# Kernel tuning notes

Hardware: AMD Instinct MI355X
Metric: run time of the kernel (lower is better)

## Reference

```python
import jax, jax.numpy as jnp
import numpy as np

N_NODES = 100000
N_EDGES = 1600000
N_GRAPHS = 512
IN_FEATS = 128
HIDDEN = 128
EXTRA = 8


def setup_inputs() -> dict:
    key = jax.random.key(0)
    ks = jax.random.split(key, 20)
    inp = {
        'feats_node': jax.random.normal(ks[0], (N_NODES, IN_FEATS), jnp.float32),
        'feats_graph': jax.random.normal(ks[1], (N_GRAPHS, EXTRA), jnp.float32),
        'edge_src': jax.random.randint(ks[2], (N_EDGES,), 0, N_NODES, jnp.int32),
        'edge_dst': jax.random.randint(ks[3], (N_EDGES,), 0, N_NODES, jnp.int32),
        'graph_ids': jnp.sort(jax.random.randint(ks[4], (N_NODES,), 0, N_GRAPHS, jnp.int32)),
        # GraphConv weights (in, out) and biases, init ~ N(0, 0.5^2) / zeros as in torch code
        'W1': 0.5 * jax.random.normal(ks[5], (IN_FEATS, HIDDEN), jnp.float32),
        'b1': jnp.zeros((HIDDEN,), jnp.float32),
        'W2': 0.5 * jax.random.normal(ks[6], (HIDDEN, HIDDEN), jnp.float32),
        'b2': jnp.zeros((HIDDEN,), jnp.float32),
        'W3': 0.5 * jax.random.normal(ks[7], (HIDDEN, HIDDEN), jnp.float32),
        'b3': jnp.zeros((HIDDEN,), jnp.float32),
        # MLP head
        'Wl1': 0.5 * jax.random.normal(ks[8], (HIDDEN + EXTRA, 2 * HIDDEN), jnp.float32),
        'bl1': jnp.zeros((2 * HIDDEN,), jnp.float32),
        'Wl2': 0.5 * jax.random.normal(ks[9], (2 * HIDDEN, HIDDEN), jnp.float32),
        'bl2': jnp.zeros((HIDDEN,), jnp.float32),
        'Wl3': 0.5 * jax.random.normal(ks[10], (HIDDEN, 1), jnp.float32),
        'bl3': jnp.zeros((1,), jnp.float32),
    }
    return inp


def _graph_conv(x, edge_src, edge_dst, norm_src, norm_dst, W, b):
    # DGL GraphConv, norm='both': D_dst^{-1/2} A D_src^{-1/2} X W + b
    h = x * norm_src[:, None]
    agg = jax.ops.segment_sum(h[edge_src], edge_dst, num_segments=N_NODES)
    agg = agg * norm_dst[:, None]
    return agg @ W + b


def reference(feats_node, feats_graph, edge_src, edge_dst, graph_ids,
              W1, b1, W2, b2, W3, b3, Wl1, bl1, Wl2, bl2, Wl3, bl3):
    ones_e = jnp.ones((N_EDGES,), jnp.float32)
    deg_out = jax.ops.segment_sum(ones_e, edge_src, num_segments=N_NODES)
    deg_in = jax.ops.segment_sum(ones_e, edge_dst, num_segments=N_NODES)
    norm_src = jnp.clip(deg_out, 1.0) ** -0.5  # out-degree norm on source side
    norm_dst = jnp.clip(deg_in, 1.0) ** -0.5   # in-degree norm on dest side

    x = jax.nn.selu(_graph_conv(feats_node, edge_src, edge_dst, norm_src, norm_dst, W1, b1))
    x = jax.nn.selu(_graph_conv(x, edge_src, edge_dst, norm_src, norm_dst, W2, b2))
    x = _graph_conv(x, edge_src, edge_dst, norm_src, norm_dst, W3, b3)

    # segment-mean readout per graph
    sums = jax.ops.segment_sum(x, graph_ids, num_segments=N_GRAPHS)
    counts = jax.ops.segment_sum(jnp.ones((N_NODES,), jnp.float32), graph_ids, num_segments=N_GRAPHS)
    embedding = sums / jnp.clip(counts, 1.0)[:, None]

    y = jnp.concatenate([embedding, feats_graph], axis=1)
    y = jax.nn.selu(y @ Wl1 + bl1)
    y = jax.nn.selu(y @ Wl2 + bl2)
    return (y @ Wl3 + bl3).reshape(-1)
```

## Files before the change

kernel.cpp:

```cpp
#include <hip/hip_runtime.h>
#include <hip/hip_fp16.h>
#include <math.h>

#define N_NODES   100000
#define N_EDGES   1600000
#define N_GRAPHS  512
#define FEAT      128
#define EXTRA     8

#define NB    196
#define PA_T  3072
#define PA_K  12

typedef _Float16 half8_t __attribute__((ext_vector_type(8)));
typedef float    f32x4_t __attribute__((ext_vector_type(4)));

static __device__ __forceinline__ float selu_f(float x){
    const float alpha = 1.6732632423543772f;
    const float scale = 1.0507009873554805f;
    return scale * (x > 0.0f ? x : alpha * expm1f(x));
}

__global__ void k_zero_i4(int4* __restrict__ p, int n4){
    int i = blockIdx.x*blockDim.x + threadIdx.x;
    if (i < n4) p[i] = make_int4(0,0,0,0);
}

__global__ __launch_bounds__(256) void k_bhist2(
        const int* __restrict__ esrc, const int* __restrict__ edst,
        int* __restrict__ bh_src, int* __restrict__ bh_dst){
    __shared__ int lhs[NB];
    __shared__ int lhd[NB];
    for (int i = threadIdx.x; i < NB; i += 256){ lhs[i] = 0; lhd[i] = 0; }
    __syncthreads();
    int stride = gridDim.x * blockDim.x;
    for (int e = blockIdx.x*blockDim.x + threadIdx.x; e < N_EDGES; e += stride){
        atomicAdd(&lhs[esrc[e] >> 9], 1);
        atomicAdd(&lhd[edst[e] >> 9], 1);
    }
    __syncthreads();
    for (int i = threadIdx.x; i < NB; i += 256){
        if (lhs[i]) atomicAdd(&bh_src[i], lhs[i]);
        if (lhd[i]) atomicAdd(&bh_dst[i], lhd[i]);
    }
}

__global__ void k_bscan2(const int* __restrict__ bh_dst, int* __restrict__ bbase,
                         int* __restrict__ gcursor, int* __restrict__ row_ptr,
                         const int* __restrict__ bh_src, int* __restrict__ sbase,
                         int* __restrict__ scursor){
    if (threadIdx.x == 0 && blockIdx.x == 0){
        int run = 0;
        for (int i = 0; i < NB; ++i){ bbase[i] = run; gcursor[i] = run; run += bh_dst[i]; }
        bbase[NB] = run;
        row_ptr[N_NODES] = N_EDGES;
        run = 0;
        for (int i = 0; i < NB; ++i){ sbase[i] = run; scursor[i] = run; run += bh_src[i]; }
        sbase[NB] = run;
    }
}

__global__ __launch_bounds__(256) void k_passA(
        const int* __restrict__ esrc, const int* __restrict__ edst,
        int* __restrict__ gcursor, uint2* __restrict__ tmp){
    __shared__ int   lcount[NB];
    __shared__ int   lscan[256];
    __shared__ int   gbase[NB];
    __shared__ ushort bid[PA_T];
    __shared__ uint2 staged[PA_T];
    __shared__ int   Vtot;
    int t = threadIdx.x;
    int base = blockIdx.x * PA_T;
    for (int i = t; i < NB; i += 256) lcount[i] = 0;
    __syncthreads();
    int bk[PA_K], slot[PA_K]; uint2 pr[PA_K];
    #pragma unroll
    for (int k = 0; k < PA_K; ++k){
        int e = base + k*256 + t;
        if (e < N_EDGES){
            int d = edst[e];
            int s = esrc[e];
            int b = d >> 9;
            bk[k] = b;
            pr[k] = make_uint2((unsigned)d, (unsigned)s);
            slot[k] = atomicAdd(&lcount[b], 1);
        } else bk[k] = -1;
    }
    __syncthreads();
    int v = (t < NB) ? lcount[t] : 0;
    lscan[t] = v;
    __syncthreads();
    for (int d = 1; d < 256; d <<= 1){
        int u = (t >= d) ? lscan[t-d] : 0;
        __syncthreads();
        lscan[t] += u;
        __syncthreads();
    }
    int excl = lscan[t] - v;
    if (t < NB) gbase[t] = atomicAdd(&gcursor[t], v);
    __syncthreads();
    lscan[t] = excl;
    if (t == 255) Vtot = excl + v;
    __syncthreads();
    #pragma unroll
    for (int k = 0; k < PA_K; ++k){
        if (bk[k] >= 0){
            int i = lscan[bk[k]] + slot[k];
            staged[i] = pr[k];
            bid[i] = (ushort)bk[k];
        }
    }
    __syncthreads();
    int total = Vtot;
    for (int i = t; i < total; i += 256){
        int b = bid[i];
        tmp[gbase[b] + (i - lscan[b])] = staged[i];
    }
}

__global__ __launch_bounds__(256) void k_passA_src(
        const int* __restrict__ esrc, int* __restrict__ scursor,
        ushort* __restrict__ tmp2){
    __shared__ int    lcount[NB];
    __shared__ int    lscan[256];
    __shared__ int    gbase[NB];
    __shared__ ushort bid[PA_T];
    __shared__ ushort staged[PA_T];
    __shared__ int    Vtot;
    int t = threadIdx.x;
    int base = blockIdx.x * PA_T;
    for (int i = t; i < NB; i += 256) lcount[i] = 0;
    __syncthreads();
    int bk[PA_K], slot[PA_K]; ushort pv[PA_K];
    #pragma unroll
    for (int k = 0; k < PA_K; ++k){
        int e = base + k*256 + t;
        if (e < N_EDGES){
            int s = esrc[e];
            int b = s >> 9;
            bk[k] = b;
            pv[k] = (ushort)(s & 511);
            slot[k] = atomicAdd(&lcount[b], 1);
        } else bk[k] = -1;
    }
    __syncthreads();
    int v = (t < NB) ? lcount[t] : 0;
    lscan[t] = v;
    __syncthreads();
    for (int d = 1; d < 256; d <<= 1){
        int u = (t >= d) ? lscan[t-d] : 0;
        __syncthreads();
        lscan[t] += u;
        __syncthreads();
    }
    int excl = lscan[t] - v;
    if (t < NB) gbase[t] = atomicAdd(&scursor[t], v);
    __syncthreads();
    lscan[t] = excl;
    if (t == 255) Vtot = excl + v;
    __syncthreads();
    #pragma unroll
    for (int k = 0; k < PA_K; ++k){
        if (bk[k] >= 0){
            int i = lscan[bk[k]] + slot[k];
            staged[i] = pv[k];
            bid[i] = (ushort)bk[k];
        }
    }
    __syncthreads();
    int total = Vtot;
    for (int i = t; i < total; i += 256){
        int b = bid[i];
        tmp2[gbase[b] + (i - lscan[b])] = staged[i];
    }
}

__global__ __launch_bounds__(256) void k_srchist(
        const ushort* __restrict__ tmp2, const int* __restrict__ sbase,
        float* __restrict__ ns){
    __shared__ int hc[512];
    int b = blockIdx.x, t = threadIdx.x;
    int node0 = b << 9;
    int lo = sbase[b], hi = sbase[b+1];
    hc[t] = 0; hc[t+256] = 0;
    __syncthreads();
    for (int p = lo + t; p < hi; p += 256)
        atomicAdd(&hc[tmp2[p]], 1);
    __syncthreads();
    int n0 = node0 + t, n1 = n0 + 256;
    if (n0 < N_NODES){ int c = hc[t];     ns[n0] = rsqrtf((float)(c > 1 ? c : 1)); }
    if (n1 < N_NODES){ int c = hc[t+256]; ns[n1] = rsqrtf((float)(c > 1 ? c : 1)); }
}

__global__ __launch_bounds__(256) void k_passB(
        const uint2* __restrict__ tmp, const int* __restrict__ bbase,
        int* __restrict__ row_ptr, int* __restrict__ col, float* __restrict__ nd){
    __shared__ int hc[512];
    __shared__ int hs[512];
    int b = blockIdx.x, t = threadIdx.x;
    int node0 = b << 9;
    int lo = bbase[b], hi = bbase[b+1];
    hc[t] = 0; hc[t+256] = 0;
    __syncthreads();
    for (int p = lo + t; p < hi; p += 256){
        int d = (int)tmp[p].x;
        atomicAdd(&hc[d - node0], 1);
    }
    __syncthreads();
    int a0 = hc[2*t], a1 = hc[2*t+1];
    int s = a0 + a1;
    hs[t] = s;
    __syncthreads();
    for (int d = 1; d < 256; d <<= 1){
        int u = (t >= d) ? hs[t-d] : 0;
        __syncthreads();
        hs[t] += u;
        __syncthreads();
    }
    int excl = hs[t] - s;
    __syncthreads();
    hs[2*t]   = excl;
    hs[2*t+1] = excl + a0;
    int n0 = node0 + 2*t, n1 = n0 + 1;
    if (n0 < N_NODES){
        row_ptr[n0] = lo + excl;
        nd[n0] = rsqrtf((float)(a0 > 1 ? a0 : 1));
    }
    if (n1 < N_NODES){
        row_ptr[n1] = lo + excl + a0;
        nd[n1] = rsqrtf((float)(a1 > 1 ? a1 : 1));
    }
    __syncthreads();
    for (int p = lo + t; p < hi; p += 256){
        uint2 e = tmp[p];
        int slot = atomicAdd(&hs[(int)e.x - node0], 1);
        col[lo + slot] = (int)e.y;
    }
}

__global__ void k_prep(const float2* __restrict__ x2, const float* __restrict__ ns,
                       __half2* __restrict__ xh2){
    int i = blockIdx.x*blockDim.x + threadIdx.x;
    if (i < N_NODES*64){
        int node = i >> 6;
        float w = ns[node];
        float2 v = x2[i];
        xh2[i] = __floats2half2_rn(v.x*w, v.y*w);
    }
}

__global__ void k_wprep(const float* __restrict__ W, __half* __restrict__ Wf){
    int i = blockIdx.x*256 + threadIdx.x;
    if (i >= 16384) return;
    int j = i & 7, lane = (i>>3) & 63, kk = (i>>9) & 3, c = i>>11;
    int k = kk*32 + ((lane>>4)<<3) + j;
    int cc = (c<<4) + (lane & 15);
    Wf[i] = __float2half(W[k*FEAT + cc]);
}

__global__ __launch_bounds__(256) void k_aggregate_h(
        const __half* __restrict__ xh, const int* __restrict__ row_ptr,
        const int* __restrict__ col, const float* __restrict__ nd,
        __half* __restrict__ outh){
    int gid  = blockIdx.x*blockDim.x + threadIdx.x;
    int node = gid >> 6;
    if (node >= N_NODES) return;
    int lane = threadIdx.x & 63;
    int sub  = lane >> 4;
    int fl   = lane & 15;
    int beg = row_ptr[node], end = row_ptr[node+1];

    float acc[8] = {0,0,0,0,0,0,0,0};
    for (int eb = beg; eb < end; eb += 16){
        int idx[4];
        uint4 r[4];
        #pragma unroll
        for (int j = 0; j < 4; ++j){
            int e = eb + 4*j + sub;
            idx[j] = (e < end) ? col[e] : -1;
        }
        #pragma unroll
        for (int j = 0; j < 4; ++j){
            r[j] = (idx[j] >= 0)
                 ? *(const uint4*)(xh + (size_t)idx[j]*FEAT + fl*8)
                 : make_uint4(0u,0u,0u,0u);
        }
        #pragma unroll
        for (int j = 0; j < 4; ++j){
            const __half2* h = (const __half2*)&r[j];
            #pragma unroll
            for (int q = 0; q < 4; ++q){
                float2 f = __half22float2(h[q]);
                acc[2*q]   += f.x;
                acc[2*q+1] += f.y;
            }
        }
    }
    #pragma unroll
    for (int q = 0; q < 8; ++q){
        acc[q] += __shfl_xor(acc[q], 16, 64);
        acc[q] += __shfl_xor(acc[q], 32, 64);
    }
    if (lane < 16){
        float wd = nd[node];
        union { __half2 h[4]; uint4 u; } pk;
        pk.h[0] = __floats2half2_rn(acc[0]*wd, acc[1]*wd);
        pk.h[1] = __floats2half2_rn(acc[2]*wd, acc[3]*wd);
        pk.h[2] = __floats2half2_rn(acc[4]*wd, acc[5]*wd);
        pk.h[3] = __floats2half2_rn(acc[6]*wd, acc[7]*wd);
        *(uint4*)(outh + (size_t)node*FEAT + fl*8) = pk.u;
    }
}

template<int ACT, int HALF_OUT>
__global__ __launch_bounds__(256) void k_gemm_mfma(
        const __half* __restrict__ A, const __half* __restrict__ Wf,
        const float* __restrict__ bias, const float* __restrict__ ns,
        float* __restrict__ fout, __half* __restrict__ hout){
    int w = threadIdx.x >> 6, lane = threadIdx.x & 63;
    int r0 = blockIdx.x*64 + w*16;
    int rl = lane & 15, kg = lane >> 4;
    int arow = r0 + rl;

    half8_t a[4];
    if (arow < N_NODES){
        const __half* ap = A + (size_t)arow*FEAT + kg*8;
        #pragma unroll
        for (int kk = 0; kk < 4; ++kk)
            a[kk] = *(const half8_t*)(ap + kk*32);
    } else {
        #pragma unroll
        for (int kk = 0; kk < 4; ++kk) a[kk] = (half8_t)(_Float16)0;
    }

    const half8_t* Bf = (const half8_t*)Wf;
    f32x4_t acc[8];
    #pragma unroll
    for (int c = 0; c < 8; ++c){
        acc[c] = (f32x4_t){0.f,0.f,0.f,0.f};
        #pragma unroll
        for (int kk = 0; kk < 4; ++kk){
            half8_t b = Bf[(c*4 + kk)*64 + lane];
            acc[c] = __builtin_amdgcn_mfma_f32_16x16x32_f16(a[kk], b, acc[c], 0, 0, 0);
        }
    }

    int orow0 = r0 + kg*4;
    float nsv[4];
    if (HALF_OUT){
        #pragma unroll
        for (int r = 0; r < 4; ++r)
            nsv[r] = (orow0 + r < N_NODES) ? ns[orow0 + r] : 0.f;
    }
    #pragma unroll
    for (int c = 0; c < 8; ++c){
        int ccol = c*16 + rl;
        float bv = bias[ccol];
        #pragma unroll
        for (int r = 0; r < 4; ++r){
            int orow = orow0 + r;
            if (orow < N_NODES){
                float v = acc[c][r] + bv;
                if (ACT) v = selu_f(v);
                if (HALF_OUT) hout[(size_t)orow*FEAT + ccol] = __float2half(v * nsv[r]);
                else          fout[(size_t)orow*FEAT + ccol] = v;
            }
        }
    }
}

__global__ void k_goff(const int* __restrict__ gid, int* __restrict__ goff){
    int g = blockIdx.x*blockDim.x + threadIdx.x;
    if (g > N_GRAPHS) return;
    if (g == N_GRAPHS){ goff[g] = N_NODES; return; }
    int lo = 0, hi = N_NODES;
    while (lo < hi){
        int mid = (lo + hi) >> 1;
        if (gid[mid] < g) lo = mid + 1; else hi = mid;
    }
    goff[g] = lo;
}

__global__ __launch_bounds__(256) void k_readout_h(
        const __half* __restrict__ ah, const int* __restrict__ goff,
        float* __restrict__ emb_part){
    __shared__ float red[16][FEAT];
    int g = blockIdx.x >> 2, c = blockIdx.x & 3;
    int t = threadIdx.x;
    int fl = t & 15, rs = t >> 4;
    int beg = goff[g], end = goff[g+1];
    int cnt = end - beg;
    int chunk = (cnt + 3) >> 2;
    int lo = beg + c*chunk;
    int hi = lo + chunk; if (hi > end) hi = end;
    float acc[8] = {0,0,0,0,0,0,0,0};
    for (int r = lo + rs; r < hi; r += 16){
        uint4 v = *(const uint4*)(ah + (size_t)r*FEAT + fl*8);
        const __half2* h = (const __half2*)&v;
        #pragma unroll
        for (int q = 0; q < 4; ++q){
            float2 f = __half22float2(h[q]);
            acc[2*q]   += f.x;
            acc[2*q+1] += f.y;
        }
    }
    #pragma unroll
    for (int q = 0; q < 8; ++q) red[rs][fl*8+q] = acc[q];
    __syncthreads();
    if (t < FEAT){
        float s = 0.f;
        #pragma unroll
        for (int i = 0; i < 16; ++i) s += red[i][t];
        emb_part[((size_t)g*4 + c)*FEAT + t] = s;
    }
}

__global__ __launch_bounds__(256) void k_mlp(
        const float* __restrict__ emb_part, const int* __restrict__ goff,
        const float* __restrict__ fg,
        const float* __restrict__ W3, const float* __restrict__ b3,
        const float* __restrict__ Wl1, const float* __restrict__ bl1,
        const float* __restrict__ Wl2, const float* __restrict__ bl2,
        const float* __restrict__ Wl3, const float* __restrict__ bl3,
        float* __restrict__ out){
    __shared__ float e[FEAT];
    __shared__ float in136[FEAT+EXTRA];
    __shared__ float y1[256];
    __shared__ float y2[128];
    int g = blockIdx.x, t = threadIdx.x;
    int cnt = goff[g+1] - goff[g]; if (cnt < 1) cnt = 1;
    float inv = 1.f / (float)cnt;
    if (t < FEAT){
        const float* p = emb_part + (size_t)g*4*FEAT;
        e[t] = (p[t] + p[FEAT+t] + p[2*FEAT+t] + p[3*FEAT+t]) * inv;
    }
    else if (t < FEAT+EXTRA + 128) {  }
    __syncthreads();
    if (t < FEAT){
        float acc = b3[t];
        for (int i = 0; i < FEAT; ++i) acc += e[i] * W3[i*FEAT + t];
        in136[t] = acc;
    } else if (t < FEAT+EXTRA){
        in136[t] = fg[g*EXTRA + (t-FEAT)];
    }
    __syncthreads();
    {
        float acc = bl1[t];
        for (int i = 0; i < FEAT+EXTRA; ++i) acc += in136[i] * Wl1[i*256 + t];
        y1[t] = selu_f(acc);
    }
    __syncthreads();
    if (t < 128){
        float acc = bl2[t];
        for (int i = 0; i < 256; ++i) acc += y1[i] * Wl2[i*128 + t];
        y2[t] = selu_f(acc);
    }
    __syncthreads();
    if (t == 0){
        float s = bl3[0];
        for (int i = 0; i < 128; ++i) s += y2[i] * Wl3[i];
        out[g] = s;
    }
}

extern "C" void kernel_launch(void* const* d_in, const int* in_sizes, int n_in,
                              void* d_out, int out_size, void* d_ws, size_t ws_size,
                              hipStream_t stream){
    const float* feats_node  = (const float*)d_in[0];
    const float* feats_graph = (const float*)d_in[1];
    const int*   edge_src    = (const int*)d_in[2];
    const int*   edge_dst    = (const int*)d_in[3];
    const int*   graph_ids   = (const int*)d_in[4];
    const float* W1 =(const float*)d_in[5];  const float* b1 =(const float*)d_in[6];
    const float* W2 =(const float*)d_in[7];  const float* b2 =(const float*)d_in[8];
    const float* W3 =(const float*)d_in[9];  const float* b3 =(const float*)d_in[10];
    const float* Wl1=(const float*)d_in[11]; const float* bl1=(const float*)d_in[12];
    const float* Wl2=(const float*)d_in[13]; const float* bl2=(const float*)d_in[14];
    const float* Wl3=(const float*)d_in[15]; const float* bl3=(const float*)d_in[16];
    float* out = (float*)d_out;
    (void)in_sizes; (void)n_in; (void)out_size; (void)ws_size;

    char* ws = (char*)d_ws;
    size_t off = 0;
    auto alloc = [&](size_t bytes)->void*{
        void* p = ws + off;
        off += (bytes + 255) & ~(size_t)255;
        return p;
    };
    __half* xh      = (__half*)alloc((size_t)N_NODES*FEAT*2);
    __half* ah      = (__half*)alloc((size_t)N_NODES*FEAT*2);
    float*  ns      = (float*) alloc((size_t)N_NODES*4);
    float*  nd      = (float*) alloc((size_t)N_NODES*4);
    int*    bhz     = (int*)   alloc((size_t)2*NB*4);
    int*    bh_src  = bhz;
    int*    bh_dst  = bhz + NB;
    int*    row_ptr = (int*)   alloc((size_t)(N_NODES+1)*4);
    int*    col     = (int*)   alloc((size_t)N_EDGES*4);
    uint2*  tmp     = (uint2*) alloc((size_t)N_EDGES*8);
    ushort* tmp2    = (ushort*)alloc((size_t)N_EDGES*2);
    int*    bbase   = (int*)   alloc((size_t)(NB+1)*4);
    int*    gcursor = (int*)   alloc((size_t)NB*4);
    int*    sbase   = (int*)   alloc((size_t)(NB+1)*4);
    int*    scursor = (int*)   alloc((size_t)NB*4);
    __half* Wf1     = (__half*)alloc((size_t)16384*2);
    __half* Wf2     = (__half*)alloc((size_t)16384*2);
    int*    goff    = (int*)   alloc((size_t)(N_GRAPHS+1)*4);
    float*  emb_part= (float*) alloc((size_t)N_GRAPHS*4*FEAT*4);

    k_zero_i4<<<dim3(1), dim3(128), 0, stream>>>((int4*)bhz, 2*NB/4);
    k_bhist2<<<dim3(512), dim3(256), 0, stream>>>(edge_src, edge_dst, bh_src, bh_dst);
    k_bscan2<<<dim3(1), dim3(64), 0, stream>>>(bh_dst, bbase, gcursor, row_ptr,
                                               bh_src, sbase, scursor);
    k_passA<<<dim3((N_EDGES + PA_T - 1)/PA_T), dim3(256), 0, stream>>>(
        edge_src, edge_dst, gcursor, tmp);
    k_passA_src<<<dim3((N_EDGES + PA_T - 1)/PA_T), dim3(256), 0, stream>>>(
        edge_src, scursor, tmp2);
    k_passB<<<dim3(NB), dim3(256), 0, stream>>>(tmp, bbase, row_ptr, col, nd);
    k_srchist<<<dim3(NB), dim3(256), 0, stream>>>(tmp2, sbase, ns);

    k_wprep<<<dim3(64), dim3(256), 0, stream>>>(W1, Wf1);
    k_wprep<<<dim3(64), dim3(256), 0, stream>>>(W2, Wf2);

    k_prep<<<dim3((N_NODES*64 + 255)/256), dim3(256), 0, stream>>>(
        (const float2*)feats_node, ns, (__half2*)xh);

    k_goff<<<dim3((N_GRAPHS+1+255)/256), dim3(256), 0, stream>>>(graph_ids, goff);

    dim3 aggGrid((N_NODES*64 + 255)/256);
    dim3 gemmGrid((N_NODES + 63)/64);
    k_aggregate_h<<<aggGrid, dim3(256), 0, stream>>>(xh, row_ptr, col, nd, ah);
    k_gemm_mfma<1,1><<<gemmGrid, dim3(256), 0, stream>>>(ah, Wf1, b1, ns, (float*)nullptr, xh);
    k_aggregate_h<<<aggGrid, dim3(256), 0, stream>>>(xh, row_ptr, col, nd, ah);
    k_gemm_mfma<1,1><<<gemmGrid, dim3(256), 0, stream>>>(ah, Wf2, b2, ns, (float*)nullptr, xh);
    k_aggregate_h<<<aggGrid, dim3(256), 0, stream>>>(xh, row_ptr, col, nd, ah);

    k_readout_h<<<dim3(N_GRAPHS*4), dim3(256), 0, stream>>>(ah, goff, emb_part);
    k_mlp<<<dim3(N_GRAPHS), dim3(256), 0, stream>>>(emb_part, goff, feats_graph,
        W3, b3, Wl1, bl1, Wl2, bl2, Wl3, bl3, out);
}
```

Before: 379.4 us.

## Accumulate aggregation in packed fp16, prescale column indices, merge weight prep

```diff
diff --git a/kernel.cpp b/kernel.cpp
--- a/kernel.cpp
+++ b/kernel.cpp
@@ -234,7 +234,7 @@
     for (int p = lo + t; p < hi; p += 256){
         uint2 e = tmp[p];
         int slot = atomicAdd(&hs[(int)e.x - node0], 1);
-        col[lo + slot] = (int)e.y;
+        col[lo + slot] = (int)(e.y << 8);
     }
 }
 
@@ -249,9 +249,12 @@
     }
 }
 
-__global__ void k_wprep(const float* __restrict__ W, __half* __restrict__ Wf){
-    int i = blockIdx.x*256 + threadIdx.x;
-    if (i >= 16384) return;
+__global__ void k_wprep2(const float* __restrict__ W1, __half* __restrict__ Wf1,
+                         const float* __restrict__ W2, __half* __restrict__ Wf2){
+    int gi = blockIdx.x*256 + threadIdx.x;
+    const float* W  = (gi < 16384) ? W1 : W2;
+    __half* Wf      = (gi < 16384) ? Wf1 : Wf2;
+    int i = gi & 16383;
     int j = i & 7, lane = (i>>3) & 63, kk = (i>>9) & 3, c = i>>11;
     int k = kk*32 + ((lane>>4)<<3) + j;
     int cc = (c<<4) + (lane & 15);
@@ -269,45 +272,51 @@
     int sub  = lane >> 4;
     int fl   = lane & 15;
     int beg = row_ptr[node], end = row_ptr[node+1];
-
-    float acc[8] = {0,0,0,0,0,0,0,0};
+    const char* base = (const char*)xh + fl*16;
+
+    __half2 acc[4];
+    #pragma unroll
+    for (int q = 0; q < 4; ++q) acc[q] = __floats2half2_rn(0.f, 0.f);
+
     for (int eb = beg; eb < end; eb += 16){
-        int idx[4];
+        int off[4];
         uint4 r[4];
         #pragma unroll
         for (int j = 0; j < 4; ++j){
             int e = eb + 4*j + sub;
-            idx[j] = (e < end) ? col[e] : -1;
+            off[j] = (e < end) ? col[e] : -1;
         }
         #pragma unroll
         for (int j = 0; j < 4; ++j){
-            r[j] = (idx[j] >= 0)
-                 ? *(const uint4*)(xh + (size_t)idx[j]*FEAT + fl*8)
+            r[j] = (off[j] >= 0)
+                 ? *(const uint4*)(base + off[j])
                  : make_uint4(0u,0u,0u,0u);
         }
         #pragma unroll
         for (int j = 0; j < 4; ++j){
             const __half2* h = (const __half2*)&r[j];
             #pragma unroll
-            for (int q = 0; q < 4; ++q){
-                float2 f = __half22float2(h[q]);
-                acc[2*q]   += f.x;
-                acc[2*q+1] += f.y;
-            }
-        }
-    }
-    #pragma unroll
-    for (int q = 0; q < 8; ++q){
-        acc[q] += __shfl_xor(acc[q], 16, 64);
-        acc[q] += __shfl_xor(acc[q], 32, 64);
+            for (int q = 0; q < 4; ++q)
+                acc[q] = __hadd2(acc[q], h[q]);
+        }
+    }
+    #pragma unroll
+    for (int q = 0; q < 4; ++q){
+        union { __half2 h; int i; } u, v;
+        u.h = acc[q];
+        v.i = __shfl_xor(u.i, 16, 64);
+        u.h = __hadd2(u.h, v.h);
+        v.i = __shfl_xor(u.i, 32, 64);
+        acc[q] = __hadd2(u.h, v.h);
     }
     if (lane < 16){
         float wd = nd[node];
         union { __half2 h[4]; uint4 u; } pk;
-        pk.h[0] = __floats2half2_rn(acc[0]*wd, acc[1]*wd);
-        pk.h[1] = __floats2half2_rn(acc[2]*wd, acc[3]*wd);
-        pk.h[2] = __floats2half2_rn(acc[4]*wd, acc[5]*wd);
-        pk.h[3] = __floats2half2_rn(acc[6]*wd, acc[7]*wd);
+        #pragma unroll
+        for (int q = 0; q < 4; ++q){
+            float2 f = __half22float2(acc[q]);
+            pk.h[q] = __floats2half2_rn(f.x*wd, f.y*wd);
+        }
         *(uint4*)(outh + (size_t)node*FEAT + fl*8) = pk.u;
     }
 }
@@ -434,7 +443,6 @@
         const float* p = emb_part + (size_t)g*4*FEAT;
         e[t] = (p[t] + p[FEAT+t] + p[2*FEAT+t] + p[3*FEAT+t]) * inv;
     }
-    else if (t < FEAT+EXTRA + 128) {  }
     __syncthreads();
     if (t < FEAT){
         float acc = b3[t];
@@ -518,8 +526,7 @@
     k_passB<<<dim3(NB), dim3(256), 0, stream>>>(tmp, bbase, row_ptr, col, nd);
     k_srchist<<<dim3(NB), dim3(256), 0, stream>>>(tmp2, sbase, ns);
 
-    k_wprep<<<dim3(64), dim3(256), 0, stream>>>(W1, Wf1);
-    k_wprep<<<dim3(64), dim3(256), 0, stream>>>(W2, Wf2);
+    k_wprep2<<<dim3(128), dim3(256), 0, stream>>>(W1, Wf1, W2, Wf2);
 
     k_prep<<<dim3((N_NODES*64 + 255)/256), dim3(256), 0, stream>>>(
         (const float2*)feats_node, ns, (__half2*)xh);
```

Result: no change. 379.6 us (+0.0%).
